# Kernel optimization log

Measured on AMD Instinct MI355X. Metric: run time of the kernel, lower is better.

Reference implementation:

```python
import jax, jax.numpy as jnp
import numpy as np

N_NODES = 50000
N_EDGES = 400000


def setup_inputs() -> dict:
    key = jax.random.key(0)
    k1, k2, k3, k4 = jax.random.split(key, 4)
    in_feat = jax.random.normal(k1, (2, 64, 4, N_NODES), dtype=jnp.float32)
    src = jax.random.randint(k2, (N_EDGES,), 0, N_NODES, dtype=jnp.int32)
    dst = jax.random.randint(k3, (N_EDGES,), 0, N_NODES, dtype=jnp.int32)
    W = jax.random.normal(k4, (64, 64), dtype=jnp.float32) * (1.0 / 8.0)
    b = jnp.zeros((64,), dtype=jnp.float32)
    return {"in_feat": in_feat, "src": src, "dst": dst, "W": W, "b": b}


def reference(in_feat, src, dst, W, b):
    # in_feat: (B, h, T, N). Net permutation [3,1,2,0] then [0,3,2,1] == [3,0,2,1]
    x = jnp.transpose(in_feat, (3, 0, 2, 1))  # (N, B, T, h) -- node-major for GraphConv
    N = x.shape[0]
    ones_e = jnp.ones(src.shape[0], dtype=x.dtype)
    deg_out = jnp.clip(jax.ops.segment_sum(ones_e, src, num_segments=N), 1.0)
    deg_in = jnp.clip(jax.ops.segment_sum(ones_e, dst, num_segments=N), 1.0)
    # DGL GraphConv, norm='both', in_feats == out_feats -> aggregate then matmul
    x = x * jax.lax.rsqrt(deg_out)[:, None, None, None]
    agg = jax.ops.segment_sum(x[src], dst, num_segments=N)  # (N, B, T, h)
    agg = agg * jax.lax.rsqrt(deg_in)[:, None, None, None]
    h = jnp.einsum('nbth,hf->nbtf', agg, W) + b
    h = jax.nn.relu(h)
    # inverse permutation [0,3,2,1] then [3,1,2,0] == transpose(h, (1,3,2,0))
    out = jnp.transpose(h, (1, 3, 2, 0))  # (B, h, T, N)
    return jax.nn.relu(out)
```

## Files before the change

kernel.cpp:

```cpp
#include <hip/hip_runtime.h>
#include <hip/hip_fp16.h>


extern "C" __global__ void k_deg(const int* __restrict__ src, const int* __restrict__ dst,
                                 int* __restrict__ deg_out, int* __restrict__ deg_in, int E) {
  int e = blockIdx.x * blockDim.x + threadIdx.x;
  if (e < E) {
    atomicAdd(&deg_out[src[e]], 1);
    atomicAdd(&deg_in[dst[e]], 1);
  }
}

extern "C" __global__ __launch_bounds__(256) void k_scan1(const int* __restrict__ deg_in,
                                                          const int* __restrict__ deg_out,
                                                          int* __restrict__ bsum,
                                                          float* __restrict__ rs_out,
                                                          float* __restrict__ rs_in, int N) {
  __shared__ int red[256];
  int tid = threadIdx.x;
  int i = blockIdx.x * 256 + tid;
  int di = (i < N) ? deg_in[i] : 0;
  red[tid] = di;
  if (i < N) {
    int a = deg_out[i] > 1 ? deg_out[i] : 1;
    int b = di > 1 ? di : 1;
    rs_out[i] = rsqrtf((float)a);
    rs_in[i]  = rsqrtf((float)b);
  }
  __syncthreads();
  #pragma unroll
  for (int off = 128; off > 0; off >>= 1) {
    if (tid < off) red[tid] += red[tid + off];
    __syncthreads();
  }
  if (tid == 0) bsum[blockIdx.x] = red[0];
}

extern "C" __global__ __launch_bounds__(256) void k_scan2(const int* __restrict__ bsum,
                                                          int* __restrict__ boffs,
                                                          int* __restrict__ offs, int M, int N) {
  __shared__ int sc[256];
  int tid = threadIdx.x;
  int v = (tid < M) ? bsum[tid] : 0;
  sc[tid] = v;
  __syncthreads();
  #pragma unroll
  for (int off = 1; off < 256; off <<= 1) {
    int t = sc[tid];
    if (tid >= off) t += sc[tid - off];
    __syncthreads();
    sc[tid] = t;
    __syncthreads();
  }
  boffs[tid] = sc[tid] - v;
  if (tid == 255) offs[N] = sc[255];
}

extern "C" __global__ __launch_bounds__(256) void k_scan3(const int* __restrict__ deg,
                                                          const int* __restrict__ boffs,
                                                          int* __restrict__ offs, int N) {
  __shared__ int sc[256];
  int tid = threadIdx.x;
  int i = blockIdx.x * 256 + tid;
  int v = (i < N) ? deg[i] : 0;
  sc[tid] = v;
  __syncthreads();
  #pragma unroll
  for (int off = 1; off < 256; off <<= 1) {
    int t = sc[tid];
    if (tid >= off) t += sc[tid - off];
    __syncthreads();
    sc[tid] = t;
    __syncthreads();
  }
  if (i < N) offs[i] = boffs[blockIdx.x] + sc[tid] - v;
}

extern "C" __global__ void k_scatter(const int* __restrict__ src, const int* __restrict__ dst,
                                     const int* __restrict__ offs, int* __restrict__ cursor,
                                     int* __restrict__ csr_src, int E) {
  int e = blockIdx.x * blockDim.x + threadIdx.x;
  if (e < E) {
    int d = dst[e];
    int pos = offs[d] + atomicAdd(&cursor[d], 1);
    csr_src[pos] = src[e];
  }
}

extern "C" __global__ __launch_bounds__(256, 2) void k_transform(
    const float* __restrict__ in_feat, const float* __restrict__ W,
    const float* __restrict__ rs_out, __half* __restrict__ y, int N) {
  int tid = threadIdx.x;
  int wave = tid >> 6, lane = tid & 63;
  int bt = blockIdx.y * 4 + wave;
  int b = bt >> 2, t = bt & 3;
  int n = blockIdx.x * 64 + lane;

  const float* xp = in_feat + (size_t)(b * 256 + t) * (size_t)N;
  size_t hstride = (size_t)4 * (size_t)N;

  float acc[64];
  #pragma unroll
  for (int f = 0; f < 64; ++f) acc[f] = 0.0f;

  bool ok = (n < N);

  float xcur[4], xnxt[4];
  #pragma unroll
  for (int u = 0; u < 4; ++u)
    xcur[u] = ok ? xp[(size_t)u * hstride + n] : 0.0f;

  #pragma unroll 1
  for (int h0 = 0; h0 < 60; h0 += 4) {
    #pragma unroll
    for (int u = 0; u < 4; ++u)
      xnxt[u] = ok ? xp[(size_t)(h0 + 4 + u) * hstride + n] : 0.0f;
    #pragma unroll
    for (int u = 0; u < 4; ++u) {
      const float* wrow = W + (h0 + u) * 64;
      #pragma unroll
      for (int f = 0; f < 64; ++f) acc[f] = fmaf(xcur[u], wrow[f], acc[f]);
    }
    #pragma unroll
    for (int u = 0; u < 4; ++u) xcur[u] = xnxt[u];
  }
  #pragma unroll
  for (int u = 0; u < 4; ++u) {
    const float* wrow = W + (60 + u) * 64;
    #pragma unroll
    for (int f = 0; f < 64; ++f) acc[f] = fmaf(xcur[u], wrow[f], acc[f]);
  }

  if (ok) {
    float rs = rs_out[n];
    union { unsigned int u[32]; uint4 v[8]; } pk;
    #pragma unroll
    for (int q = 0; q < 32; ++q) {
      __half2 h2 = __float22half2_rn(make_float2(acc[2 * q] * rs, acc[2 * q + 1] * rs));
      pk.u[q] = *(unsigned int*)&h2;
    }
    uint4* yp = (uint4*)(y + (size_t)n * 512 + bt * 64);
    #pragma unroll
    for (int q = 0; q < 8; ++q) yp[q] = pk.v[q];
  }
}

extern "C" __global__ __launch_bounds__(512) void k_aggregate(
    const __half* __restrict__ y, const int* __restrict__ offs,
    const int* __restrict__ csr_src, const float* __restrict__ rs_in,
    const float* __restrict__ bvec, float* __restrict__ out, int N) {
  __shared__ float agg[16 * 513];
  int tid = threadIdx.x;
  int lane = tid & 63, wave = tid >> 6;
  int n0 = blockIdx.x * 16;

#define ACC_EDGE(s)                                                          \
  {                                                                          \
    const uint2* rp = (const uint2*)(y + (size_t)(s) * 512);                 \
    uint2 ua = rp[lane];                                                     \
    uint2 ub = rp[64 + lane];                                                \
    float2 f;                                                                \
    f = __half22float2(*(const __half2*)&ua.x); accA.x += f.x; accA.y += f.y;\
    f = __half22float2(*(const __half2*)&ua.y); accA.z += f.x; accA.w += f.y;\
    f = __half22float2(*(const __half2*)&ub.x); accB.x += f.x; accB.y += f.y;\
    f = __half22float2(*(const __half2*)&ub.y); accB.z += f.x; accB.w += f.y;\
  }

  #pragma unroll
  for (int k = 0; k < 2; ++k) {
    int nl = k * 8 + wave;
    int n = n0 + nl;
    float4 accA = {0.f, 0.f, 0.f, 0.f};
    float4 accB = {0.f, 0.f, 0.f, 0.f};
    if (n < N) {
      int j0 = offs[n], j1 = offs[n + 1];
      for (int base = j0; base < j1; base += 64) {
        int idxv = csr_src[base + lane];
        int m = j1 - base; if (m > 64) m = 64;
        int e = 0;
        for (; e + 3 < m; e += 4) {
          int s0 = __builtin_amdgcn_readlane(idxv, e);
          int s1 = __builtin_amdgcn_readlane(idxv, e + 1);
          int s2 = __builtin_amdgcn_readlane(idxv, e + 2);
          int s3 = __builtin_amdgcn_readlane(idxv, e + 3);
          ACC_EDGE(s0); ACC_EDGE(s1); ACC_EDGE(s2); ACC_EDGE(s3);
        }
        for (; e < m; ++e) {
          int s0 = __builtin_amdgcn_readlane(idxv, e);
          ACC_EDGE(s0);
        }
      }
    }
    *(float4*)&agg[nl * 513 + lane * 4] = accA;
    *(float4*)&agg[nl * 513 + 256 + lane * 4] = accB;
  }
#undef ACC_EDGE
  __syncthreads();

  int nl = tid & 15;
  int r0 = tid >> 4;
  int n = n0 + nl;
  float rs = (n < N) ? rs_in[n] : 0.0f;
  #pragma unroll 4
  for (int it = 0; it < 16; ++it) {
    int c = it * 32 + r0;
    float v = agg[nl * 513 + c];
    int f = c & 63, bt = c >> 6;
    int b = bt >> 2, t = bt & 3;
    v = v * rs + bvec[f];
    v = fmaxf(v, 0.0f);
    if (n < N) out[(size_t)((b * 64 + f) * 4 + t) * (size_t)N + n] = v;
  }
}

extern "C" void kernel_launch(void* const* d_in, const int* in_sizes, int n_in,
                              void* d_out, int out_size, void* d_ws, size_t ws_size,
                              hipStream_t stream) {
  const float* in_feat = (const float*)d_in[0];
  const int*   src     = (const int*)d_in[1];
  const int*   dst     = (const int*)d_in[2];
  const float* W       = (const float*)d_in[3];
  const float* bvec    = (const float*)d_in[4];
  float* out = (float*)d_out;

  int N = in_sizes[0] / 512;
  int E = in_sizes[1];

  int A  = (N + 64) & ~63;
  int EA = (E + 63) & ~63;
  int M  = (N + 255) / 256;

  int*   deg_out_i = (int*)d_ws;
  int*   deg_in_i  = deg_out_i + A;
  int*   cursor    = deg_in_i + A;
  int*   offs      = cursor + A;
  int*   bsum      = offs + A;
  int*   boffs     = bsum + 256;
  float* rs_out    = (float*)(boffs + 256);
  float* rs_in     = rs_out + A;
  int*   csr_src   = (int*)(rs_in + A);
  __half* y        = (__half*)(csr_src + EA);

  hipMemsetAsync(deg_out_i, 0, (size_t)(3 * A) * sizeof(int), stream);
  hipLaunchKernelGGL(k_deg, dim3((E + 255) / 256), dim3(256), 0, stream,
                     src, dst, deg_out_i, deg_in_i, E);
  hipLaunchKernelGGL(k_scan1, dim3(M), dim3(256), 0, stream,
                     deg_in_i, deg_out_i, bsum, rs_out, rs_in, N);
  hipLaunchKernelGGL(k_scan2, dim3(1), dim3(256), 0, stream, bsum, boffs, offs, M, N);
  hipLaunchKernelGGL(k_scan3, dim3(M), dim3(256), 0, stream, deg_in_i, boffs, offs, N);
  hipLaunchKernelGGL(k_scatter, dim3((E + 255) / 256), dim3(256), 0, stream,
                     src, dst, offs, cursor, csr_src, E);
  hipLaunchKernelGGL(k_transform, dim3((N + 63) / 64, 2, 1), dim3(256), 0, stream,
                     in_feat, W, rs_out, y, N);
  hipLaunchKernelGGL(k_aggregate, dim3((N + 15) / 16), dim3(512), 0, stream,
                     y, offs, csr_src, rs_in, bvec, out, N);
}
```

Baseline: 206.0 us.

## Use MFMA f16 matrix cores for the per-node feature transform

Rewrites the transform kernel so each wave computes 16-node tiles with __builtin_amdgcn_mfma_f32_16x16x32_f16 instead of 64 scalar FMA accumulators per thread. Inputs are scaled by rs_out and converted to fp16 before the matmul, and W fragments are held in registers. This removes the scalar FMA cost and the register pressure of the old kernel. In exchange, inputs are rounded to fp16 before the multiply, the in_feat loads are only 16 nodes wide, and y is written with scattered 2-byte stores.

```diff
diff --git a/kernel.cpp b/kernel.cpp
--- a/kernel.cpp
+++ b/kernel.cpp
@@ -1,6 +1,9 @@
 #include <hip/hip_runtime.h>
 #include <hip/hip_fp16.h>
 
+
+typedef _Float16 half8 __attribute__((ext_vector_type(8)));
+typedef float f32x4 __attribute__((ext_vector_type(4)));
 
 extern "C" __global__ void k_deg(const int* __restrict__ src, const int* __restrict__ dst,
                                  int* __restrict__ deg_out, int* __restrict__ deg_in, int E) {
@@ -87,61 +90,62 @@
   }
 }
 
-extern "C" __global__ __launch_bounds__(256, 2) void k_transform(
+extern "C" __global__ __launch_bounds__(256) void k_transform(
     const float* __restrict__ in_feat, const float* __restrict__ W,
     const float* __restrict__ rs_out, __half* __restrict__ y, int N) {
   int tid = threadIdx.x;
-  int wave = tid >> 6, lane = tid & 63;
-  int bt = blockIdx.y * 4 + wave;
-  int b = bt >> 2, t = bt & 3;
-  int n = blockIdx.x * 64 + lane;
-
-  const float* xp = in_feat + (size_t)(b * 256 + t) * (size_t)N;
-  size_t hstride = (size_t)4 * (size_t)N;
-
-  float acc[64];
-  #pragma unroll
-  for (int f = 0; f < 64; ++f) acc[f] = 0.0f;
-
-  bool ok = (n < N);
-
-  float xcur[4], xnxt[4];
-  #pragma unroll
-  for (int u = 0; u < 4; ++u)
-    xcur[u] = ok ? xp[(size_t)u * hstride + n] : 0.0f;
-
-  #pragma unroll 1
-  for (int h0 = 0; h0 < 60; h0 += 4) {
-    #pragma unroll
-    for (int u = 0; u < 4; ++u)
-      xnxt[u] = ok ? xp[(size_t)(h0 + 4 + u) * hstride + n] : 0.0f;
-    #pragma unroll
-    for (int u = 0; u < 4; ++u) {
-      const float* wrow = W + (h0 + u) * 64;
+  int wave = tid >> 6, l = tid & 63;
+  int col = l & 15;
+  int kg  = l >> 4;
+  int n0 = blockIdx.x * 16;
+
+  half8 wf[4][2];
+  #pragma unroll
+  for (int ft = 0; ft < 4; ++ft)
+    #pragma unroll
+    for (int ks = 0; ks < 2; ++ks)
       #pragma unroll
-      for (int f = 0; f < 64; ++f) acc[f] = fmaf(xcur[u], wrow[f], acc[f]);
+      for (int j = 0; j < 8; ++j)
+        wf[ft][ks][j] = (_Float16)W[(ks * 32 + kg * 8 + j) * 64 + ft * 16 + col];
+
+  int nA = n0 + col;
+  bool okA = (nA < N);
+  float rs = okA ? rs_out[nA] : 0.0f;
+  size_t hs = (size_t)4 * (size_t)N;
+
+  #pragma unroll
+  for (int p = 0; p < 2; ++p) {
+    int bt = wave * 2 + p;
+    int b = bt >> 2, t = bt & 3;
+    const float* xp = in_feat + (size_t)(b * 256 + t) * (size_t)N + nA;
+
+    float a0f[8], a1f[8];
+    #pragma unroll
+    for (int j = 0; j < 8; ++j)
+      a0f[j] = okA ? xp[(size_t)(kg * 8 + j) * hs] : 0.0f;
+    #pragma unroll
+    for (int j = 0; j < 8; ++j)
+      a1f[j] = okA ? xp[(size_t)(32 + kg * 8 + j) * hs] : 0.0f;
+
+    half8 a0, a1;
+    #pragma unroll
+    for (int j = 0; j < 8; ++j) {
+      a0[j] = (_Float16)(a0f[j] * rs);
+      a1[j] = (_Float16)(a1f[j] * rs);
     }
-    #pragma unroll
-    for (int u = 0; u < 4; ++u) xcur[u] = xnxt[u];
-  }
-  #pragma unroll
-  for (int u = 0; u < 4; ++u) {
-    const float* wrow = W + (60 + u) * 64;
-    #pragma unroll
-    for (int f = 0; f < 64; ++f) acc[f] = fmaf(xcur[u], wrow[f], acc[f]);
-  }
-
-  if (ok) {
-    float rs = rs_out[n];
-    union { unsigned int u[32]; uint4 v[8]; } pk;
-    #pragma unroll
-    for (int q = 0; q < 32; ++q) {
-      __half2 h2 = __float22half2_rn(make_float2(acc[2 * q] * rs, acc[2 * q + 1] * rs));
-      pk.u[q] = *(unsigned int*)&h2;
+
+    #pragma unroll
+    for (int ft = 0; ft < 4; ++ft) {
+      f32x4 acc = {0.f, 0.f, 0.f, 0.f};
+      acc = __builtin_amdgcn_mfma_f32_16x16x32_f16(a0, wf[ft][0], acc, 0, 0, 0);
+      acc = __builtin_amdgcn_mfma_f32_16x16x32_f16(a1, wf[ft][1], acc, 0, 0, 0);
+      #pragma unroll
+      for (int r = 0; r < 4; ++r) {
+        int nr = n0 + kg * 4 + r;
+        if (nr < N)
+          y[(size_t)nr * 512 + bt * 64 + ft * 16 + col] = __float2half(acc[r]);
+      }
     }
-    uint4* yp = (uint4*)(y + (size_t)n * 512 + bt * 64);
-    #pragma unroll
-    for (int q = 0; q < 8; ++q) yp[q] = pk.v[q];
   }
 }
 
@@ -250,7 +254,7 @@
   hipLaunchKernelGGL(k_scan3, dim3(M), dim3(256), 0, stream, deg_in_i, boffs, offs, N);
   hipLaunchKernelGGL(k_scatter, dim3((E + 255) / 256), dim3(256), 0, stream,
                      src, dst, offs, cursor, csr_src, E);
-  hipLaunchKernelGGL(k_transform, dim3((N + 63) / 64, 2, 1), dim3(256), 0, stream,
+  hipLaunchKernelGGL(k_transform, dim3((N + 15) / 16), dim3(256), 0, stream,
                      in_feat, W, rs_out, y, N);
   hipLaunchKernelGGL(k_aggregate, dim3((N + 15) / 16), dim3(512), 0, stream,
                      y, offs, csr_src, rs_in, bvec, out, N);
```

After: 184.1 us. -10.6%, faster.
